# Kernel optimization log

Measured on AMD Instinct MI355X. Metric: run time of the kernel, lower is better.

## Reference

```python
import jax, jax.numpy as jnp
import numpy as np


def setup_inputs() -> dict:
    key = jax.random.key(0)
    k1, k2, k3 = jax.random.split(key, 3)
    N, C, S = 8192, 256, 7
    D = C * S * S            # 12544 flattened RoI feature dim
    NUM_CLASSES = 81         # includes background (softmax cls head)
    x = jax.random.normal(k1, (N, C, S, S), dtype=jnp.float32)
    # fc weights ~ N(0, 0.01) like mmdet's normal init
    W_cls = jax.random.normal(k2, (NUM_CLASSES, D), dtype=jnp.float32) * 0.01
    b_cls = jnp.zeros((NUM_CLASSES,), dtype=jnp.float32)
    W_reg = jax.random.normal(k3, (4 * NUM_CLASSES, D), dtype=jnp.float32) * 0.001
    b_reg = jnp.zeros((4 * NUM_CLASSES,), dtype=jnp.float32)
    return {"x": x, "W_cls": W_cls, "b_cls": b_cls, "W_reg": W_reg, "b_reg": b_reg}


def reference(x, W_cls, b_cls, W_reg, b_reg):
    # BBoxHead.forward: flatten RoI features, then cls / reg FC heads.
    N = x.shape[0]
    feat = x.reshape(N, -1)                      # [N, C*S*S]
    cls_score = feat @ W_cls.T + b_cls           # [N, num_classes]
    bbox_pred = feat @ W_reg.T + b_reg           # [N, 4*num_classes]
    return cls_score, bbox_pred
```

## Files before the change

### kernel.cpp

```cpp
#include <hip/hip_runtime.h>
#include <stdint.h>
#include <stddef.h>

#define K_FULL 12544
#define M_ROWS 8192
#define NCLS 81
#define NREG 324
#define NTOT 405
#define NPAD 416
#define OUT0 663552
#define OUT_TOTAL 3317760

typedef __bf16 bf16x8 __attribute__((ext_vector_type(8)));
typedef float floatx4 __attribute__((ext_vector_type(4)));

__device__ __forceinline__ uint32_t pack2_bf16(float a, float b) {
  uint32_t ua = __float_as_uint(a);
  uint32_t ub = __float_as_uint(b);
  ua = (ua + 0x7FFFu + ((ua >> 16) & 1u)) >> 16;
  ub = (ub + 0x7FFFu + ((ub >> 16) & 1u)) >> 16;
  return ua | (ub << 16);
}

__global__ void pack_w(const float* __restrict__ Wc, const float* __restrict__ Wr,
                       uint16_t* __restrict__ Wb) {
  const int u = blockIdx.x * blockDim.x + threadIdx.x;
  if (u >= (K_FULL / 8)) return;
  const int row = blockIdx.y;
  uint4 v = {0u, 0u, 0u, 0u};
  const float* src = nullptr;
  if (row < NCLS) src = Wc + (size_t)row * K_FULL;
  else if (row < NTOT) src = Wr + (size_t)(row - NCLS) * K_FULL;
  if (src) {
    const float4 f0 = *(const float4*)(src + u * 8);
    const float4 f1 = *(const float4*)(src + u * 8 + 4);
    v.x = pack2_bf16(f0.x, f0.y);
    v.y = pack2_bf16(f0.z, f0.w);
    v.z = pack2_bf16(f1.x, f1.y);
    v.w = pack2_bf16(f1.z, f1.w);
  }
  *(uint4*)(Wb + (size_t)row * K_FULL + u * 8) = v;
}

__global__ void bias_init(const float* __restrict__ bc, const float* __restrict__ br,
                          float* __restrict__ out) {
  const int i = blockIdx.x * blockDim.x + threadIdx.x;
  if (i >= OUT_TOTAL) return;
  if (i < OUT0) {
    out[i] = bc[i % NCLS];
  } else {
    const int j = i - OUT0;
    out[i] = br[j % NREG];
  }
}

__global__ __launch_bounds__(512, 2) void gemm_kernel(
    const float* __restrict__ x, const uint16_t* __restrict__ Wb,
    float* __restrict__ out) {
  __shared__ uint4 sA4[1024];
  __shared__ uint4 sB4[3328];
  uint8_t* sA = (uint8_t*)sA4;
  uint8_t* sB = (uint8_t*)sB4;

  const int tid = threadIdx.x;
  const int lane = tid & 63;
  const int wave = tid >> 6;
  const int mg = wave >> 1;
  const int ng = wave & 1;

  const int mt = blockIdx.x >> 2;
  const int ks = blockIdx.x & 3;
  const int rowBase = mt * 128;
  int k0 = ks * 3136;
  const int kEnd = k0 + 3136;

  floatx4 acc[2][13];
  const floatx4 zero = {0.0f, 0.0f, 0.0f, 0.0f};
#pragma unroll
  for (int i = 0; i < 2; ++i)
#pragma unroll
    for (int j = 0; j < 13; ++j) acc[i][j] = zero;

  const int rB = lane >> 3;
  const int pB = lane & 7;

  for (; k0 < kEnd; k0 += 64) {
    __syncthreads();

#pragma unroll
    for (int i = 0; i < 2; ++i) {
      const int U = tid + i * 512;
      const int m = U >> 3;
      const int p = U & 7;
      const int kb = p ^ (m & 7);
      const float* g = x + (size_t)(rowBase + m) * K_FULL + (k0 + kb * 8);
      const float4 f0 = *(const float4*)g;
      const float4 f1 = *(const float4*)(g + 4);
      uint4 v;
      v.x = pack2_bf16(f0.x, f0.y);
      v.y = pack2_bf16(f0.z, f0.w);
      v.z = pack2_bf16(f1.x, f1.y);
      v.w = pack2_bf16(f1.z, f1.w);
      *(uint4*)(sA + m * 128 + p * 16) = v;
    }

    for (int i = wave; i < 52; i += 8) {
      const int n = i * 8 + rB;
      const int kb = pB ^ (n & 7);
      const uint16_t* g = Wb + (size_t)n * K_FULL + (k0 + kb * 8);
      __builtin_amdgcn_global_load_lds(
          (const __attribute__((address_space(1))) void*)g,
          (__attribute__((address_space(3))) void*)(sB + i * 1024), 16, 0, 0);
    }

    __syncthreads();

#pragma unroll
    for (int s = 0; s < 2; ++s) {
      const int q = lane >> 4;
      const int kb = s * 4 + q;
      const int m0 = mg * 32 + (lane & 15);
      const int m1 = m0 + 16;
      const bf16x8 a0 = *(const bf16x8*)(sA + m0 * 128 + ((kb ^ (m0 & 7)) * 16));
      const bf16x8 a1 = *(const bf16x8*)(sA + m1 * 128 + ((kb ^ (m1 & 7)) * 16));
#pragma unroll
      for (int nf = 0; nf < 13; ++nf) {
        const int n = ng * 208 + nf * 16 + (lane & 15);
        const bf16x8 b = *(const bf16x8*)(sB + n * 128 + ((kb ^ (n & 7)) * 16));
        acc[0][nf] = __builtin_amdgcn_mfma_f32_16x16x32_bf16(a0, b, acc[0][nf], 0, 0, 0);
        acc[1][nf] = __builtin_amdgcn_mfma_f32_16x16x32_bf16(a1, b, acc[1][nf], 0, 0, 0);
      }
    }
  }

  const int q = lane >> 4;
  const int c0 = lane & 15;
#pragma unroll
  for (int fm = 0; fm < 2; ++fm) {
    const int r0 = rowBase + mg * 32 + fm * 16 + q * 4;
#pragma unroll
    for (int nf = 0; nf < 13; ++nf) {
      const int col = ng * 208 + nf * 16 + c0;
      if (col < NCLS) {
        float* dst = out + (size_t)r0 * NCLS + col;
#pragma unroll
        for (int r = 0; r < 4; ++r)
          unsafeAtomicAdd(dst + (size_t)r * NCLS, acc[fm][nf][r]);
      } else if (col < NTOT) {
        float* dst = out + OUT0 + (size_t)r0 * NREG + (col - NCLS);
#pragma unroll
        for (int r = 0; r < 4; ++r)
          unsafeAtomicAdd(dst + (size_t)r * NREG, acc[fm][nf][r]);
      }
    }
  }
}

extern "C" void kernel_launch(void* const* d_in, const int* in_sizes, int n_in,
                              void* d_out, int out_size, void* d_ws, size_t ws_size,
                              hipStream_t stream) {
  const float* x = (const float*)d_in[0];
  const float* Wc = (const float*)d_in[1];
  const float* bc = (const float*)d_in[2];
  const float* Wr = (const float*)d_in[3];
  const float* br = (const float*)d_in[4];
  float* out = (float*)d_out;
  uint16_t* Wb = (uint16_t*)d_ws;

  pack_w<<<dim3(7, 416), dim3(256), 0, stream>>>(Wc, Wr, Wb);
  bias_init<<<dim3((OUT_TOTAL + 255) / 256), dim3(256), 0, stream>>>(bc, br, out);
  gemm_kernel<<<dim3(256), dim3(512), 0, stream>>>(x, Wb, out);
}
```

Measured before the change: 703.7 us.

## Halve M tile to 64 rows, double grid, and register-prefetch next A tile

The GEMM block tile shrinks from 128 to 64 rows, so the grid doubles to 512 blocks and the launch bounds allow 4 blocks per CU, with one accumulator row-fragment per wave. The fp32 x loads for the next k-step are issued into registers right after the barrier, overlapping global latency with the MFMA loop. The aim is more parallelism and latency hiding on a grid that previously had only 256 blocks. The cost is that each W tile is reloaded twice as often per row, which raises LDS and L2 traffic for B, and the extra blocks add atomic contention.

```diff
diff --git a/kernel.cpp b/kernel.cpp
--- a/kernel.cpp
+++ b/kernel.cpp
@@ -54,10 +54,10 @@
   }
 }
 
-__global__ __launch_bounds__(512, 2) void gemm_kernel(
+__global__ __launch_bounds__(512, 4) void gemm_kernel(
     const float* __restrict__ x, const uint16_t* __restrict__ Wb,
     float* __restrict__ out) {
-  __shared__ uint4 sA4[1024];
+  __shared__ uint4 sA4[512];
   __shared__ uint4 sB4[3328];
   uint8_t* sA = (uint8_t*)sA4;
   uint8_t* sB = (uint8_t*)sB4;
@@ -70,44 +70,43 @@
 
   const int mt = blockIdx.x >> 2;
   const int ks = blockIdx.x & 3;
-  const int rowBase = mt * 128;
+  const int rowBase = mt * 64;
   int k0 = ks * 3136;
   const int kEnd = k0 + 3136;
 
-  floatx4 acc[2][13];
+  floatx4 acc[13];
   const floatx4 zero = {0.0f, 0.0f, 0.0f, 0.0f};
 #pragma unroll
-  for (int i = 0; i < 2; ++i)
-#pragma unroll
-    for (int j = 0; j < 13; ++j) acc[i][j] = zero;
+  for (int j = 0; j < 13; ++j) acc[j] = zero;
+
+  const int mA = tid >> 3;
+  const int pA = tid & 7;
+  const int kbA = pA ^ (mA & 7);
+  const float* gA = x + (size_t)(rowBase + mA) * K_FULL + k0 + kbA * 8;
 
   const int rB = lane >> 3;
   const int pB = lane & 7;
+  const int kbB = pB ^ rB;
+
+  float4 pf0 = *(const float4*)gA;
+  float4 pf1 = *(const float4*)(gA + 4);
+  gA += 64;
 
   for (; k0 < kEnd; k0 += 64) {
     __syncthreads();
 
-#pragma unroll
-    for (int i = 0; i < 2; ++i) {
-      const int U = tid + i * 512;
-      const int m = U >> 3;
-      const int p = U & 7;
-      const int kb = p ^ (m & 7);
-      const float* g = x + (size_t)(rowBase + m) * K_FULL + (k0 + kb * 8);
-      const float4 f0 = *(const float4*)g;
-      const float4 f1 = *(const float4*)(g + 4);
+    {
       uint4 v;
-      v.x = pack2_bf16(f0.x, f0.y);
-      v.y = pack2_bf16(f0.z, f0.w);
-      v.z = pack2_bf16(f1.x, f1.y);
-      v.w = pack2_bf16(f1.z, f1.w);
-      *(uint4*)(sA + m * 128 + p * 16) = v;
+      v.x = pack2_bf16(pf0.x, pf0.y);
+      v.y = pack2_bf16(pf0.z, pf0.w);
+      v.z = pack2_bf16(pf1.x, pf1.y);
+      v.w = pack2_bf16(pf1.z, pf1.w);
+      *(uint4*)(sA + mA * 128 + pA * 16) = v;
     }
 
     for (int i = wave; i < 52; i += 8) {
       const int n = i * 8 + rB;
-      const int kb = pB ^ (n & 7);
-      const uint16_t* g = Wb + (size_t)n * K_FULL + (k0 + kb * 8);
+      const uint16_t* g = Wb + (size_t)n * K_FULL + (k0 + kbB * 8);
       __builtin_amdgcn_global_load_lds(
           (const __attribute__((address_space(1))) void*)g,
           (__attribute__((address_space(3))) void*)(sB + i * 1024), 16, 0, 0);
@@ -115,43 +114,43 @@
 
     __syncthreads();
 
+    if (k0 + 64 < kEnd) {
+      pf0 = *(const float4*)gA;
+      pf1 = *(const float4*)(gA + 4);
+      gA += 64;
+    }
+
+    const int q = lane >> 4;
+    const int m0 = mg * 16 + (lane & 15);
 #pragma unroll
     for (int s = 0; s < 2; ++s) {
-      const int q = lane >> 4;
       const int kb = s * 4 + q;
-      const int m0 = mg * 32 + (lane & 15);
-      const int m1 = m0 + 16;
       const bf16x8 a0 = *(const bf16x8*)(sA + m0 * 128 + ((kb ^ (m0 & 7)) * 16));
-      const bf16x8 a1 = *(const bf16x8*)(sA + m1 * 128 + ((kb ^ (m1 & 7)) * 16));
 #pragma unroll
       for (int nf = 0; nf < 13; ++nf) {
         const int n = ng * 208 + nf * 16 + (lane & 15);
         const bf16x8 b = *(const bf16x8*)(sB + n * 128 + ((kb ^ (n & 7)) * 16));
-        acc[0][nf] = __builtin_amdgcn_mfma_f32_16x16x32_bf16(a0, b, acc[0][nf], 0, 0, 0);
-        acc[1][nf] = __builtin_amdgcn_mfma_f32_16x16x32_bf16(a1, b, acc[1][nf], 0, 0, 0);
+        acc[nf] = __builtin_amdgcn_mfma_f32_16x16x32_bf16(a0, b, acc[nf], 0, 0, 0);
       }
     }
   }
 
   const int q = lane >> 4;
   const int c0 = lane & 15;
+  const int r0 = rowBase + mg * 16 + q * 4;
 #pragma unroll
-  for (int fm = 0; fm < 2; ++fm) {
-    const int r0 = rowBase + mg * 32 + fm * 16 + q * 4;
+  for (int nf = 0; nf < 13; ++nf) {
+    const int col = ng * 208 + nf * 16 + c0;
+    if (col < NCLS) {
+      float* dst = out + (size_t)r0 * NCLS + col;
 #pragma unroll
-    for (int nf = 0; nf < 13; ++nf) {
-      const int col = ng * 208 + nf * 16 + c0;
-      if (col < NCLS) {
-        float* dst = out + (size_t)r0 * NCLS + col;
+      for (int r = 0; r < 4; ++r)
+        unsafeAtomicAdd(dst + (size_t)r * NCLS, acc[nf][r]);
+    } else if (col < NTOT) {
+      float* dst = out + OUT0 + (size_t)r0 * NREG + (col - NCLS);
 #pragma unroll
-        for (int r = 0; r < 4; ++r)
-          unsafeAtomicAdd(dst + (size_t)r * NCLS, acc[fm][nf][r]);
-      } else if (col < NTOT) {
-        float* dst = out + OUT0 + (size_t)r0 * NREG + (col - NCLS);
-#pragma unroll
-        for (int r = 0; r < 4; ++r)
-          unsafeAtomicAdd(dst + (size_t)r * NREG, acc[fm][nf][r]);
-      }
+      for (int r = 0; r < 4; ++r)
+        unsafeAtomicAdd(dst + (size_t)r * NREG, acc[nf][r]);
     }
   }
 }
@@ -169,5 +168,5 @@
 
   pack_w<<<dim3(7, 416), dim3(256), 0, stream>>>(Wc, Wr, Wb);
   bias_init<<<dim3((OUT_TOTAL + 255) / 256), dim3(256), 0, stream>>>(bc, br, out);
-  gemm_kernel<<<dim3(256), dim3(512), 0, stream>>>(x, Wb, out);
+  gemm_kernel<<<dim3(512), dim3(512), 0, stream>>>(x, Wb, out);
 }
```

After: 657.8 us. -6.5%, faster.
